# Optimization experiments

Hardware: AMD Instinct MI355X
Metric: run time of the kernel (lower is better)

## Reference

```python
import jax, jax.numpy as jnp
import numpy as np

B, C1, D1, C2, D2 = 128, 1152, 8, 10, 16
ROUTING_ITERS = 3


def squash(s, axis=-1, eps=1e-8):
    # squash(s) = (|s|^2 / (1+|s|^2)) * s / sqrt(|s|^2 + eps)
    sq = jnp.sum(s * s, axis=axis, keepdims=True)
    return (sq / (1.0 + sq)) * s / jnp.sqrt(sq + eps)


def setup_inputs() -> dict:
    key = jax.random.key(0)
    k1, k2, k3 = jax.random.split(key, 3)
    inputs = jax.random.normal(k1, (B, C1 * D1), dtype=jnp.float32)
    # W: (caps1, caps2, d2, d1), truncated normal stddev=0.1 (leading batch-1 dim dropped)
    W = jax.random.truncated_normal(k2, -2.0, 2.0, (C1, C2, D2, D1), dtype=jnp.float32) * 0.1
    # routing bias: (1, 1, caps2, d2)
    bias = jax.random.normal(k3, (1, 1, C2, D2), dtype=jnp.float32) * 0.1
    return {"inputs": inputs, "W": W, "bias": bias}


def reference(inputs, W, bias):
    b = inputs.shape[0]
    # PrimaryCaps: reshape to [B, C1, D1] then squash over the capsule dim (axis=-2 of
    # the original [B, C1, 1, D1, 1] tensor == D1 here)
    prim = squash(inputs.reshape(b, C1, D1), axis=-1)
    # DigitalCaps (fast): u_hat[b,i,j,:] = W[i,j] @ prim[b,i]  -> [B, C1, C2, D2]
    u_hat = jnp.einsum('cjdk,bck->bcjd', W, prim)
    u_stop = jax.lax.stop_gradient(u_hat)
    raw = jnp.zeros((b, C1, C2, 1), dtype=inputs.dtype)
    v = None
    for r in range(ROUTING_ITERS):
        u = u_hat if r == ROUTING_ITERS - 1 else u_stop
        c = jax.nn.softmax(raw, axis=2)                      # softmax over output caps
        s = jnp.sum(c * u, axis=1, keepdims=True) + bias     # [B, 1, C2, D2]
        v = squash(s, axis=-1)                               # squash over D2 (orig axis=-2)
        if r != ROUTING_ITERS - 1:
            # agreement: sum over D2 of u * v (v broadcasts over C1)
            raw = raw + jnp.sum(u * v, axis=-1, keepdims=True)
    # original returns [B, 1, C2, D2, 1]
    return v[..., None]
```

## Files before the change

### kernel.cpp

```cpp
#include <hip/hip_runtime.h>
#include <hip/hip_fp16.h>

#define BATCH 128
#define NC1   1152
#define ND1   8
#define NC2   10
#define ND2   16
#define SDIM  (NC2 * ND2)

#define CB 16
#define BB 32

__device__ __forceinline__ unsigned pack_h2(float a, float b) {
    __half2 h = __floats2half2_rn(a, b);
    return *reinterpret_cast<unsigned*>(&h);
}
__device__ __forceinline__ float2 unpack_h2(unsigned v) {
    __half2 h = *reinterpret_cast<__half2*>(&v);
    return __half22float2(h);
}
__device__ __forceinline__ unsigned pmul_h2(unsigned a, unsigned b) {
    __half2 ha = *reinterpret_cast<__half2*>(&a);
    __half2 hb = *reinterpret_cast<__half2*>(&b);
    __half2 r = __hmul2(ha, hb);
    return *reinterpret_cast<unsigned*>(&r);
}
__device__ __forceinline__ unsigned padd_h2(unsigned a, unsigned b) {
    __half2 ha = *reinterpret_cast<__half2*>(&a);
    __half2 hb = *reinterpret_cast<__half2*>(&b);
    __half2 r = __hadd2(ha, hb);
    return *reinterpret_cast<unsigned*>(&r);
}

template<int CTRL>
__device__ __forceinline__ unsigned dpp_mov(unsigned v) {
    return (unsigned)__builtin_amdgcn_mov_dpp((int)v, CTRL, 0xF, 0xF, true);
}
__device__ __forceinline__ unsigned row_reduce_h2(unsigned t2) {
    t2 = padd_h2(t2, dpp_mov<0x128>(t2));
    t2 = padd_h2(t2, dpp_mov<0x124>(t2));
    t2 = padd_h2(t2, dpp_mov<0x122>(t2));
    t2 = padd_h2(t2, dpp_mov<0x121>(t2));
    return t2;
}

__global__ void caps_zero(float* __restrict__ s0) {
    s0[blockIdx.x * 256 + threadIdx.x] = 0.0f;
}

__global__ __launch_bounds__(256, 1) void caps_uhat(
    const float* __restrict__ x,
    const float* __restrict__ W,
    unsigned* __restrict__ u_ws,
    float* __restrict__ s0)
{
    const int cb  = blockIdx.x;
    const int bb  = blockIdx.y;
    const int tid = threadIdx.x;
    const int cl  = tid >> 4;
    const int d   = tid & 15;
    const int wl  = tid & 63;

    __shared__ float prim[BB][CB][ND1];

    for (int i = tid; i < BB * CB; i += 256) {
        const int b = i >> 4, c = i & 15;
        const float* xr = x + ((size_t)(bb * BB + b) * NC1 + (cb * CB + c)) * ND1;
        float4 a0 = *(const float4*)(xr);
        float4 a1 = *(const float4*)(xr + 4);
        float sq = a0.x*a0.x + a0.y*a0.y + a0.z*a0.z + a0.w*a0.w
                 + a1.x*a1.x + a1.y*a1.y + a1.z*a1.z + a1.w*a1.w;
        float g = (sq / (1.0f + sq)) * rsqrtf(sq + 1e-8f);
        prim[b][c][0] = a0.x * g; prim[b][c][1] = a0.y * g;
        prim[b][c][2] = a0.z * g; prim[b][c][3] = a0.w * g;
        prim[b][c][4] = a1.x * g; prim[b][c][5] = a1.y * g;
        prim[b][c][6] = a1.z * g; prim[b][c][7] = a1.w * g;
    }
    __syncthreads();

    const int c_glob = cb * CB + cl;
    float w[NC2][ND1];
    #pragma unroll
    for (int j = 0; j < NC2; ++j) {
        const float* Wr = W + (((size_t)c_glob * NC2 + j) * ND2 + d) * ND1;
        float4 w0 = *(const float4*)(Wr);
        float4 w1 = *(const float4*)(Wr + 4);
        w[j][0] = w0.x; w[j][1] = w0.y; w[j][2] = w0.z; w[j][3] = w0.w;
        w[j][4] = w1.x; w[j][5] = w1.y; w[j][6] = w1.z; w[j][7] = w1.w;
    }

    for (int k = 0; k < BB; ++k) {
        const int b = (k + cb) & (BB - 1);
        const int bglob = bb * BB + b;
        float p[ND1];
        #pragma unroll
        for (int kk = 0; kk < ND1; ++kk) p[kk] = prim[b][cl][kk];

        unsigned* ur = u_ws + ((size_t)bglob * 5 * NC1 + c_glob) * 16 + d;
        #pragma unroll
        for (int jp = 0; jp < 5; ++jp) {
            float u0 = 0.f, u1 = 0.f;
            #pragma unroll
            for (int kk = 0; kk < ND1; ++kk) {
                u0 += w[2*jp  ][kk] * p[kk];
                u1 += w[2*jp+1][kk] * p[kk];
            }
            unsigned pk = pack_h2(u0, u1);
            ur[(size_t)jp * (NC1 * 16)] = pk;
            pk = padd_h2(pk, (unsigned)__shfl_xor((int)pk, 16));
            pk = padd_h2(pk, (unsigned)__shfl_xor((int)pk, 32));
            if (wl < 16) {
                float2 f = unpack_h2(pk);
                atomicAdd(&s0[(size_t)bglob * SDIM + (2*jp)   * 16 + d], f.x);
                atomicAdd(&s0[(size_t)bglob * SDIM + (2*jp+1) * 16 + d], f.y);
            }
        }
    }
}

__global__ __launch_bounds__(512, 1) void caps_pass(
    const unsigned* __restrict__ u_ws,
    const float* __restrict__ sv,
    const float* __restrict__ bias,
    float* __restrict__ spart,
    int mode)
{
    const int bx   = blockIdx.x;
    const int b    = bx >> 2;
    const int q    = bx & 3;
    const int tid  = threadIdx.x;
    const int grp  = tid >> 4;
    const int d    = tid & 15;
    const int wave = tid >> 6;

    __shared__ float vl[SDIM];
    __shared__ float sred[8][SDIM];

    if (tid < SDIM) {
        float s = sv[(size_t)b * SDIM + tid];
        if (mode == 0) {
            s = 0.1f * s + bias[tid];
            float sq = s * s;
            sq += __shfl_xor(sq, 1); sq += __shfl_xor(sq, 2);
            sq += __shfl_xor(sq, 4); sq += __shfl_xor(sq, 8);
            s = (sq / (1.0f + sq)) * rsqrtf(sq + 1e-8f) * s;
        }
        vl[tid] = s;
    }
    __syncthreads();

    unsigned vsf[5];
    #pragma unroll
    for (int jp = 0; jp < 5; ++jp)
        vsf[jp] = pack_h2(vl[(2*jp)*16 + d], vl[(2*jp+1)*16 + d]);

    const unsigned* ub = u_ws + (size_t)b * 5 * NC1 * 16 + d;
    const int c0 = q * 288 + grp;

    float sp[NC2];
    #pragma unroll
    for (int j = 0; j < NC2; ++j) sp[j] = 0.0f;

    unsigned o[5], on[5];
    #pragma unroll
    for (int jp = 0; jp < 5; ++jp)
        o[jp] = ub[(size_t)jp * (NC1 * 16) + (size_t)c0 * 16];

    for (int i = 0; i < 9; ++i) {
        if (i + 1 < 9) {
            const int c = c0 + (i + 1) * 32;
            #pragma unroll
            for (int jp = 0; jp < 5; ++jp)
                on[jp] = ub[(size_t)jp * (NC1 * 16) + (size_t)c * 16];
        }
        float u[NC2], r[NC2];
        #pragma unroll
        for (int jp = 0; jp < 5; ++jp) {
            float2 f = unpack_h2(o[jp]);
            u[2*jp] = f.x; u[2*jp+1] = f.y;
            unsigned t2 = row_reduce_h2(pmul_h2(o[jp], vsf[jp]));
            float2 rr = unpack_h2(t2);
            r[2*jp] = rr.x; r[2*jp+1] = rr.y;
        }
        float ssum = 0.0f;
        #pragma unroll
        for (int j = 0; j < NC2; ++j) { r[j] = __expf(r[j]); ssum += r[j]; }
        float inv = 1.0f / ssum;
        #pragma unroll
        for (int j = 0; j < NC2; ++j) sp[j] += (r[j] * inv) * u[j];
        #pragma unroll
        for (int jp = 0; jp < 5; ++jp) o[jp] = on[jp];
    }

    #pragma unroll
    for (int j = 0; j < NC2; ++j) {
        sp[j] += __shfl_xor(sp[j], 16);
        sp[j] += __shfl_xor(sp[j], 32);
    }
    if ((tid & 63) < 16) {
        #pragma unroll
        for (int j = 0; j < NC2; ++j) sred[wave][j * 16 + d] = sp[j];
    }
    __syncthreads();
    if (tid < SDIM) {
        float acc = 0.0f;
        #pragma unroll
        for (int w = 0; w < 8; ++w) acc += sred[w][tid];
        spart[((size_t)b * 4 + q) * SDIM + tid] = acc;
    }
}

__global__ void caps_comb1(const float* __restrict__ s0,
                           const float* __restrict__ spart,
                           const float* __restrict__ bias,
                           float* __restrict__ v) {
    const int b = blockIdx.x, tid = threadIdx.x;
    if (tid >= SDIM) return;
    float bv = bias[tid];
    float s_a = 0.1f * s0[(size_t)b * SDIM + tid] + bv;
    float s_b = spart[((size_t)b * 4 + 0) * SDIM + tid]
              + spart[((size_t)b * 4 + 1) * SDIM + tid]
              + spart[((size_t)b * 4 + 2) * SDIM + tid]
              + spart[((size_t)b * 4 + 3) * SDIM + tid] + bv;
    float qa = s_a * s_a;
    qa += __shfl_xor(qa, 1); qa += __shfl_xor(qa, 2);
    qa += __shfl_xor(qa, 4); qa += __shfl_xor(qa, 8);
    float qb = s_b * s_b;
    qb += __shfl_xor(qb, 1); qb += __shfl_xor(qb, 2);
    qb += __shfl_xor(qb, 4); qb += __shfl_xor(qb, 8);
    float v0 = (qa / (1.0f + qa)) * rsqrtf(qa + 1e-8f) * s_a;
    float v1 = (qb / (1.0f + qb)) * rsqrtf(qb + 1e-8f) * s_b;
    v[(size_t)b * SDIM + tid] = v0 + v1;
}

__global__ void caps_comb2(const float* __restrict__ spart,
                           const float* __restrict__ bias,
                           float* __restrict__ out) {
    const int b = blockIdx.x, tid = threadIdx.x;
    if (tid >= SDIM) return;
    float s = spart[((size_t)b * 4 + 0) * SDIM + tid]
            + spart[((size_t)b * 4 + 1) * SDIM + tid]
            + spart[((size_t)b * 4 + 2) * SDIM + tid]
            + spart[((size_t)b * 4 + 3) * SDIM + tid] + bias[tid];
    float sq = s * s;
    sq += __shfl_xor(sq, 1); sq += __shfl_xor(sq, 2);
    sq += __shfl_xor(sq, 4); sq += __shfl_xor(sq, 8);
    out[(size_t)b * SDIM + tid] = (sq / (1.0f + sq)) * rsqrtf(sq + 1e-8f) * s;
}

__global__ __launch_bounds__(1024) void caps_fused(
    const float* __restrict__ x, const float* __restrict__ W,
    const float* __restrict__ bias, float* __restrict__ out)
{
    const int b    = blockIdx.x;
    const int tid  = threadIdx.x;
    const int grp  = tid >> 4;
    const int d    = tid & 15;
    const int wave = tid >> 6;
    const int lane = tid & 63;

    __shared__ float prim[NC1][ND1];
    __shared__ float sred[16][SDIM];
    __shared__ float vbuf[SDIM];

    const float* xb = x + (size_t)b * (NC1 * ND1);
    for (int c = tid; c < NC1; c += 1024) {
        float4 a0 = *(const float4*)(xb + c * 8);
        float4 a1 = *(const float4*)(xb + c * 8 + 4);
        float sq = a0.x*a0.x + a0.y*a0.y + a0.z*a0.z + a0.w*a0.w
                 + a1.x*a1.x + a1.y*a1.y + a1.z*a1.z + a1.w*a1.w;
        float g = (sq / (1.0f + sq)) * rsqrtf(sq + 1e-8f);
        prim[c][0] = a0.x * g; prim[c][1] = a0.y * g;
        prim[c][2] = a0.z * g; prim[c][3] = a0.w * g;
        prim[c][4] = a1.x * g; prim[c][5] = a1.y * g;
        prim[c][6] = a1.z * g; prim[c][7] = a1.w * g;
    }
    __syncthreads();

    float vsum[NC2], sp[NC2];
    for (int pass = 0; pass < 3; ++pass) {
        #pragma unroll
        for (int j = 0; j < NC2; ++j) sp[j] = 0.0f;
        for (int c = grp; c < NC1; c += 64) {
            float p[8];
            #pragma unroll
            for (int k = 0; k < 8; ++k) p[k] = prim[c][k];
            const float* Wc = W + (size_t)c * (NC2 * ND2 * ND1) + d * ND1;
            float u[NC2];
            #pragma unroll
            for (int j = 0; j < NC2; ++j) {
                const float4 w0 = *(const float4*)(Wc + j * (ND2 * ND1));
                const float4 w1 = *(const float4*)(Wc + j * (ND2 * ND1) + 4);
                u[j] = w0.x*p[0] + w0.y*p[1] + w0.z*p[2] + w0.w*p[3]
                     + w1.x*p[4] + w1.y*p[5] + w1.z*p[6] + w1.w*p[7];
            }
            if (pass == 0) {
                #pragma unroll
                for (int j = 0; j < NC2; ++j) sp[j] += u[j];
            } else {
                float r[NC2];
                #pragma unroll
                for (int j = 0; j < NC2; ++j) {
                    float t = u[j] * vsum[j];
                    t += __shfl_xor(t, 1); t += __shfl_xor(t, 2);
                    t += __shfl_xor(t, 4); t += __shfl_xor(t, 8);
                    r[j] = t;
                }
                float m = r[0];
                #pragma unroll
                for (int j = 1; j < NC2; ++j) m = fmaxf(m, r[j]);
                float ssum = 0.0f;
                #pragma unroll
                for (int j = 0; j < NC2; ++j) { r[j] = __expf(r[j] - m); ssum += r[j]; }
                float inv = 1.0f / ssum;
                #pragma unroll
                for (int j = 0; j < NC2; ++j) sp[j] += (r[j] * inv) * u[j];
            }
        }
        #pragma unroll
        for (int j = 0; j < NC2; ++j) {
            sp[j] += __shfl_xor(sp[j], 16);
            sp[j] += __shfl_xor(sp[j], 32);
        }
        if (lane < 16) {
            #pragma unroll
            for (int j = 0; j < NC2; ++j) sred[wave][j * 16 + d] = sp[j];
        }
        __syncthreads();
        if (tid < SDIM) {
            float acc = 0.0f;
            #pragma unroll
            for (int w = 0; w < 16; ++w) acc += sred[w][tid];
            float s = bias[tid] + (pass == 0 ? 0.1f * acc : acc);
            float sq = s * s;
            sq += __shfl_xor(sq, 1); sq += __shfl_xor(sq, 2);
            sq += __shfl_xor(sq, 4); sq += __shfl_xor(sq, 8);
            float vv = (sq / (1.0f + sq)) * rsqrtf(sq + 1e-8f) * s;
            if (pass == 2) out[(size_t)b * SDIM + tid] = vv;
            else           vbuf[tid] = vv;
        }
        __syncthreads();
        if (pass < 2) {
            #pragma unroll
            for (int j = 0; j < NC2; ++j) {
                float vv = vbuf[j * 16 + d];
                vsum[j] = (pass == 0) ? vv : (vsum[j] + vv);
            }
        }
        __syncthreads();
    }
}

extern "C" void kernel_launch(void* const* d_in, const int* in_sizes, int n_in,
                              void* d_out, int out_size, void* d_ws, size_t ws_size,
                              hipStream_t stream) {
    const float* x    = (const float*)d_in[0];
    const float* W    = (const float*)d_in[1];
    const float* bias = (const float*)d_in[2];
    float* out = (float*)d_out;

    const size_t u_bytes  = (size_t)BATCH * 5 * NC1 * 16 * 4;
    const size_t s0_bytes = (size_t)BATCH * SDIM * 4;
    const size_t v_bytes  = (size_t)BATCH * SDIM * 4;
    const size_t sp_bytes = (size_t)BATCH * 4 * SDIM * 4;
    const size_t need = u_bytes + s0_bytes + v_bytes + sp_bytes;

    if (ws_size >= need) {
        unsigned* u_ws  = (unsigned*)d_ws;
        float*    s0    = (float*)((char*)d_ws + u_bytes);
        float*    v     = (float*)((char*)d_ws + u_bytes + s0_bytes);
        float*    spart = (float*)((char*)d_ws + u_bytes + s0_bytes + v_bytes);

        caps_zero <<<80, 256, 0, stream>>>(s0);
        caps_uhat <<<dim3(NC1 / CB, BATCH / BB), 256, 0, stream>>>(x, W, u_ws, s0);
        caps_pass <<<BATCH * 4, 512, 0, stream>>>(u_ws, s0, bias, spart, 0);
        caps_comb1<<<BATCH, 192, 0, stream>>>(s0, spart, bias, v);
        caps_pass <<<BATCH * 4, 512, 0, stream>>>(u_ws, v, bias, spart, 1);
        caps_comb2<<<BATCH, 192, 0, stream>>>(spart, bias, out);
    } else {
        caps_fused<<<BATCH, 1024, 0, stream>>>(x, W, bias, out);
    }
}
```

Measured before the change: 70.22 us.

## Fold combine step into routing pass, split capsules six ways, halve uhat registers

The separate comb1 kernel is removed, and each caps_pass block now recomputes v from s0 and the previous pass's partial sums itself, which saves one launch and one global round trip. Input capsules are split into 6 chunks per batch instead of 4, so more blocks run in each pass. The u_hat kernel loads W in two halves (3 and 2 pairs of output capsules) to cut register pressure, which allows 2 blocks per CU. In exchange, every pass block redundantly recomputes the squash, and the u_hat kernel now runs the batch loop twice, rereading prim from shared memory.

```diff
diff --git a/kernel.cpp b/kernel.cpp
--- a/kernel.cpp
+++ b/kernel.cpp
@@ -11,6 +11,10 @@
 #define CB 16
 #define BB 32
 
+#define NQ   6
+#define QCAP (NC1 / NQ)
+#define CPGP (QCAP / 32)
+
 __device__ __forceinline__ unsigned pack_h2(float a, float b) {
     __half2 h = __floats2half2_rn(a, b);
     return *reinterpret_cast<unsigned*>(&h);
@@ -48,7 +52,58 @@
     s0[blockIdx.x * 256 + threadIdx.x] = 0.0f;
 }
 
-__global__ __launch_bounds__(256, 1) void caps_uhat(
+template<int JP0, int NJP>
+__device__ __forceinline__ void uhat_half(
+    const float* __restrict__ W, unsigned* __restrict__ u_ws,
+    float* __restrict__ s0, const float (*prim)[CB][ND1],
+    int cb, int bb, int c_glob, int cl, int d, int wl)
+{
+    float w[NJP][2][8];
+    #pragma unroll
+    for (int t = 0; t < NJP; ++t) {
+        #pragma unroll
+        for (int jj = 0; jj < 2; ++jj) {
+            const int j = 2 * (JP0 + t) + jj;
+            const float* Wr = W + (((size_t)c_glob * NC2 + j) * ND2 + d) * ND1;
+            float4 w0 = *(const float4*)(Wr);
+            float4 w1 = *(const float4*)(Wr + 4);
+            w[t][jj][0] = w0.x; w[t][jj][1] = w0.y;
+            w[t][jj][2] = w0.z; w[t][jj][3] = w0.w;
+            w[t][jj][4] = w1.x; w[t][jj][5] = w1.y;
+            w[t][jj][6] = w1.z; w[t][jj][7] = w1.w;
+        }
+    }
+    for (int k = 0; k < BB; ++k) {
+        const int b = (k + cb) & (BB - 1);
+        const int bglob = bb * BB + b;
+        float p[ND1];
+        #pragma unroll
+        for (int kk = 0; kk < ND1; ++kk) p[kk] = prim[b][cl][kk];
+
+        unsigned* ur = u_ws + ((size_t)bglob * 5 * NC1 + c_glob) * 16 + d;
+        #pragma unroll
+        for (int t = 0; t < NJP; ++t) {
+            const int jp = JP0 + t;
+            float u0 = 0.f, u1 = 0.f;
+            #pragma unroll
+            for (int kk = 0; kk < ND1; ++kk) {
+                u0 += w[t][0][kk] * p[kk];
+                u1 += w[t][1][kk] * p[kk];
+            }
+            unsigned pk = pack_h2(u0, u1);
+            ur[(size_t)jp * (NC1 * 16)] = pk;
+            pk = padd_h2(pk, (unsigned)__shfl_xor((int)pk, 16));
+            pk = padd_h2(pk, (unsigned)__shfl_xor((int)pk, 32));
+            if (wl < 16) {
+                float2 f = unpack_h2(pk);
+                atomicAdd(&s0[(size_t)bglob * SDIM + (2*jp)   * 16 + d], f.x);
+                atomicAdd(&s0[(size_t)bglob * SDIM + (2*jp+1) * 16 + d], f.y);
+            }
+        }
+    }
+}
+
+__global__ __launch_bounds__(256, 2) void caps_uhat(
     const float* __restrict__ x,
     const float* __restrict__ W,
     unsigned* __restrict__ u_ws,
@@ -79,55 +134,21 @@
     __syncthreads();
 
     const int c_glob = cb * CB + cl;
-    float w[NC2][ND1];
-    #pragma unroll
-    for (int j = 0; j < NC2; ++j) {
-        const float* Wr = W + (((size_t)c_glob * NC2 + j) * ND2 + d) * ND1;
-        float4 w0 = *(const float4*)(Wr);
-        float4 w1 = *(const float4*)(Wr + 4);
-        w[j][0] = w0.x; w[j][1] = w0.y; w[j][2] = w0.z; w[j][3] = w0.w;
-        w[j][4] = w1.x; w[j][5] = w1.y; w[j][6] = w1.z; w[j][7] = w1.w;
-    }
-
-    for (int k = 0; k < BB; ++k) {
-        const int b = (k + cb) & (BB - 1);
-        const int bglob = bb * BB + b;
-        float p[ND1];
-        #pragma unroll
-        for (int kk = 0; kk < ND1; ++kk) p[kk] = prim[b][cl][kk];
-
-        unsigned* ur = u_ws + ((size_t)bglob * 5 * NC1 + c_glob) * 16 + d;
-        #pragma unroll
-        for (int jp = 0; jp < 5; ++jp) {
-            float u0 = 0.f, u1 = 0.f;
-            #pragma unroll
-            for (int kk = 0; kk < ND1; ++kk) {
-                u0 += w[2*jp  ][kk] * p[kk];
-                u1 += w[2*jp+1][kk] * p[kk];
-            }
-            unsigned pk = pack_h2(u0, u1);
-            ur[(size_t)jp * (NC1 * 16)] = pk;
-            pk = padd_h2(pk, (unsigned)__shfl_xor((int)pk, 16));
-            pk = padd_h2(pk, (unsigned)__shfl_xor((int)pk, 32));
-            if (wl < 16) {
-                float2 f = unpack_h2(pk);
-                atomicAdd(&s0[(size_t)bglob * SDIM + (2*jp)   * 16 + d], f.x);
-                atomicAdd(&s0[(size_t)bglob * SDIM + (2*jp+1) * 16 + d], f.y);
-            }
-        }
-    }
+    uhat_half<0, 3>(W, u_ws, s0, prim, cb, bb, c_glob, cl, d, wl);
+    uhat_half<3, 2>(W, u_ws, s0, prim, cb, bb, c_glob, cl, d, wl);
 }
 
 __global__ __launch_bounds__(512, 1) void caps_pass(
     const unsigned* __restrict__ u_ws,
-    const float* __restrict__ sv,
+    const float* __restrict__ s0,
+    const float* __restrict__ spart_in,
     const float* __restrict__ bias,
-    float* __restrict__ spart,
+    float* __restrict__ spart_out,
     int mode)
 {
     const int bx   = blockIdx.x;
-    const int b    = bx >> 2;
-    const int q    = bx & 3;
+    const int b    = bx / NQ;
+    const int q    = bx % NQ;
     const int tid  = threadIdx.x;
     const int grp  = tid >> 4;
     const int d    = tid & 15;
@@ -137,15 +158,23 @@
     __shared__ float sred[8][SDIM];
 
     if (tid < SDIM) {
-        float s = sv[(size_t)b * SDIM + tid];
-        if (mode == 0) {
-            s = 0.1f * s + bias[tid];
-            float sq = s * s;
-            sq += __shfl_xor(sq, 1); sq += __shfl_xor(sq, 2);
-            sq += __shfl_xor(sq, 4); sq += __shfl_xor(sq, 8);
-            s = (sq / (1.0f + sq)) * rsqrtf(sq + 1e-8f) * s;
-        }
-        vl[tid] = s;
+        float bv = bias[tid];
+        float s_a = 0.1f * s0[(size_t)b * SDIM + tid] + bv;
+        float qa = s_a * s_a;
+        qa += __shfl_xor(qa, 1); qa += __shfl_xor(qa, 2);
+        qa += __shfl_xor(qa, 4); qa += __shfl_xor(qa, 8);
+        float v = (qa / (1.0f + qa)) * rsqrtf(qa + 1e-8f) * s_a;
+        if (mode == 1) {
+            float s_b = bv;
+            #pragma unroll
+            for (int qq = 0; qq < NQ; ++qq)
+                s_b += spart_in[((size_t)b * NQ + qq) * SDIM + tid];
+            float qb = s_b * s_b;
+            qb += __shfl_xor(qb, 1); qb += __shfl_xor(qb, 2);
+            qb += __shfl_xor(qb, 4); qb += __shfl_xor(qb, 8);
+            v += (qb / (1.0f + qb)) * rsqrtf(qb + 1e-8f) * s_b;
+        }
+        vl[tid] = v;
     }
     __syncthreads();
 
@@ -155,7 +184,7 @@
         vsf[jp] = pack_h2(vl[(2*jp)*16 + d], vl[(2*jp+1)*16 + d]);
 
     const unsigned* ub = u_ws + (size_t)b * 5 * NC1 * 16 + d;
-    const int c0 = q * 288 + grp;
+    const int c0 = q * QCAP + grp;
 
     float sp[NC2];
     #pragma unroll
@@ -166,8 +195,8 @@
     for (int jp = 0; jp < 5; ++jp)
         o[jp] = ub[(size_t)jp * (NC1 * 16) + (size_t)c0 * 16];
 
-    for (int i = 0; i < 9; ++i) {
-        if (i + 1 < 9) {
+    for (int i = 0; i < CPGP; ++i) {
+        if (i + 1 < CPGP) {
             const int c = c0 + (i + 1) * 32;
             #pragma unroll
             for (int jp = 0; jp < 5; ++jp)
@@ -206,31 +235,8 @@
         float acc = 0.0f;
         #pragma unroll
         for (int w = 0; w < 8; ++w) acc += sred[w][tid];
-        spart[((size_t)b * 4 + q) * SDIM + tid] = acc;
-    }
-}
-
-__global__ void caps_comb1(const float* __restrict__ s0,
-                           const float* __restrict__ spart,
-                           const float* __restrict__ bias,
-                           float* __restrict__ v) {
-    const int b = blockIdx.x, tid = threadIdx.x;
-    if (tid >= SDIM) return;
-    float bv = bias[tid];
-    float s_a = 0.1f * s0[(size_t)b * SDIM + tid] + bv;
-    float s_b = spart[((size_t)b * 4 + 0) * SDIM + tid]
-              + spart[((size_t)b * 4 + 1) * SDIM + tid]
-              + spart[((size_t)b * 4 + 2) * SDIM + tid]
-              + spart[((size_t)b * 4 + 3) * SDIM + tid] + bv;
-    float qa = s_a * s_a;
-    qa += __shfl_xor(qa, 1); qa += __shfl_xor(qa, 2);
-    qa += __shfl_xor(qa, 4); qa += __shfl_xor(qa, 8);
-    float qb = s_b * s_b;
-    qb += __shfl_xor(qb, 1); qb += __shfl_xor(qb, 2);
-    qb += __shfl_xor(qb, 4); qb += __shfl_xor(qb, 8);
-    float v0 = (qa / (1.0f + qa)) * rsqrtf(qa + 1e-8f) * s_a;
-    float v1 = (qb / (1.0f + qb)) * rsqrtf(qb + 1e-8f) * s_b;
-    v[(size_t)b * SDIM + tid] = v0 + v1;
+        spart_out[((size_t)b * NQ + q) * SDIM + tid] = acc;
+    }
 }
 
 __global__ void caps_comb2(const float* __restrict__ spart,
@@ -238,10 +244,10 @@
                            float* __restrict__ out) {
     const int b = blockIdx.x, tid = threadIdx.x;
     if (tid >= SDIM) return;
-    float s = spart[((size_t)b * 4 + 0) * SDIM + tid]
-            + spart[((size_t)b * 4 + 1) * SDIM + tid]
-            + spart[((size_t)b * 4 + 2) * SDIM + tid]
-            + spart[((size_t)b * 4 + 3) * SDIM + tid] + bias[tid];
+    float s = bias[tid];
+    #pragma unroll
+    for (int q = 0; q < NQ; ++q)
+        s += spart[((size_t)b * NQ + q) * SDIM + tid];
     float sq = s * s;
     sq += __shfl_xor(sq, 1); sq += __shfl_xor(sq, 2);
     sq += __shfl_xor(sq, 4); sq += __shfl_xor(sq, 8);
@@ -361,22 +367,20 @@
 
     const size_t u_bytes  = (size_t)BATCH * 5 * NC1 * 16 * 4;
     const size_t s0_bytes = (size_t)BATCH * SDIM * 4;
-    const size_t v_bytes  = (size_t)BATCH * SDIM * 4;
-    const size_t sp_bytes = (size_t)BATCH * 4 * SDIM * 4;
-    const size_t need = u_bytes + s0_bytes + v_bytes + sp_bytes;
+    const size_t sp_bytes = (size_t)BATCH * NQ * SDIM * 4;
+    const size_t need = u_bytes + s0_bytes + 2 * sp_bytes;
 
     if (ws_size >= need) {
         unsigned* u_ws  = (unsigned*)d_ws;
         float*    s0    = (float*)((char*)d_ws + u_bytes);
-        float*    v     = (float*)((char*)d_ws + u_bytes + s0_bytes);
-        float*    spart = (float*)((char*)d_ws + u_bytes + s0_bytes + v_bytes);
+        float*    sp1   = (float*)((char*)d_ws + u_bytes + s0_bytes);
+        float*    sp2   = (float*)((char*)d_ws + u_bytes + s0_bytes + sp_bytes);
 
         caps_zero <<<80, 256, 0, stream>>>(s0);
         caps_uhat <<<dim3(NC1 / CB, BATCH / BB), 256, 0, stream>>>(x, W, u_ws, s0);
-        caps_pass <<<BATCH * 4, 512, 0, stream>>>(u_ws, s0, bias, spart, 0);
-        caps_comb1<<<BATCH, 192, 0, stream>>>(s0, spart, bias, v);
-        caps_pass <<<BATCH * 4, 512, 0, stream>>>(u_ws, v, bias, spart, 1);
-        caps_comb2<<<BATCH, 192, 0, stream>>>(spart, bias, out);
+        caps_pass <<<BATCH * NQ, 512, 0, stream>>>(u_ws, s0, sp1, bias, sp1, 0);
+        caps_pass <<<BATCH * NQ, 512, 0, stream>>>(u_ws, s0, sp1, bias, sp2, 1);
+        caps_comb2<<<BATCH, 192, 0, stream>>>(sp2, bias, out);
     } else {
         caps_fused<<<BATCH, 1024, 0, stream>>>(x, W, bias, out);
     }
```

Result: slower. 81.94 us (+16.7%).
